# Optimization experiments

Measured on AMD Instinct MI355X. Metric: run time of the kernel, lower is better.

Reference implementation:

```python
import jax, jax.numpy as jnp
import numpy as np

S, B, NS, NC = 128, 64, 128, 8
D, Z, H, HI, NF = 32, 64, 128, 128, 2
N = NS * B
LOG2PI = float(np.log(2.0 * np.pi))
_m_in = np.arange(1, Z + 1)
_m_hid = (np.arange(HI) % (Z - 1)) + 1
MASK1 = jnp.asarray((_m_hid[None, :] >= _m_in[:, None]).astype(np.float32))  # [Z,HI]
MASK2 = jnp.asarray((_m_in[None, :] > _m_hid[:, None]).astype(np.float32))   # [HI,Z]


def setup_inputs() -> dict:
    key = jax.random.key(0)
    ks = jax.random.split(key, 16)
    r = lambda i, shape: jax.random.normal(ks[i], shape, jnp.float32) * 0.1
    return dict(
        input=jax.random.normal(ks[0], (S, B, D), jnp.float32),
        eps=jax.random.normal(ks[1], (S, N, Z), jnp.float32),
        u=jax.random.uniform(ks[2], (S, 3, NC, NS, B), dtype=jnp.float32),
        Wxh=r(3, (D, H)), Wzh=r(4, (Z, H)), bh=jnp.zeros(H, jnp.float32),
        Wg=r(5, (H, Z)), bg=jnp.zeros(Z, jnp.float32),
        Wp=r(6, (H, Z)), bp=jnp.zeros(Z, jnp.float32),
        Wz=r(7, (Z, Z)), bz=jnp.zeros(Z, jnp.float32),
        Wsc=r(8, (Z, Z)), bsc=jnp.zeros(Z, jnp.float32),
        iaf_W1=r(9, (NF, Z, HI)), iaf_b1=jnp.zeros((NF, HI), jnp.float32),
        iaf_Wm=r(10, (NF, HI, Z)), iaf_bm=jnp.zeros((NF, Z), jnp.float32),
        iaf_Ws=r(11, (NF, HI, Z)), iaf_bs=jnp.zeros((NF, Z), jnp.float32),
        We1=r(12, (Z, H)), be1=jnp.zeros(H, jnp.float32),
        We2=r(13, (H, 4 * NC)), be2=jnp.zeros(4 * NC, jnp.float32),
    )


def _forward(input, eps, u, Wxh, Wzh, bh, Wg, bg, Wp, bp, Wz, bz, Wsc, bsc,
             iaf_W1, iaf_b1, iaf_Wm, iaf_bm, iaf_Ws, iaf_bs, We1, be1, We2, be2):
    def step(z_prev, inp):
        x, eps_t, u_t = inp                        # x:[B,D] eps_t:[N,Z] u_t:[3,NC,NS,B]
        xr = jnp.tile(x, (NS, 1))                  # == input[i].repeat(n_samples, 1) -> [N,D]
        # GatedTransition
        h = jax.nn.relu(xr @ Wxh + z_prev @ Wzh + bh)
        gate = jax.nn.sigmoid(h @ Wg + bg)
        prop = h @ Wp + bp
        loc = (1.0 - gate) * (z_prev @ Wz + bz) + gate * prop
        scale = jax.nn.softplus(jax.nn.relu(prop) @ Wsc + bsc) + 1e-3
        # base rsample + log_prob of base sample (eps form)
        z = loc + scale * eps_t
        base_lp = jnp.sum(-0.5 * eps_t * eps_t - jnp.log(scale) - 0.5 * LOG2PI, axis=-1)
        # IAF stack: y = sigma*x + (1-sigma)*mu, cached log_prob = base_lp - sum log sigma
        logdet = jnp.zeros((N,), z.dtype)
        for f in range(NF):
            hh = jax.nn.relu(z @ (iaf_W1[f] * MASK1) + iaf_b1[f])
            mu = hh @ (iaf_Wm[f] * MASK2) + iaf_bm[f]
            sg = jax.nn.sigmoid(hh @ (iaf_Ws[f] * MASK2) + iaf_bs[f] + 1.0)
            z = sg * z + (1.0 - sg) * mu
            logdet = logdet + jnp.sum(jnp.log(sg), axis=-1)
        z_lp = (base_lp - logdet).reshape(NS, B)
        # Emitter -> [N, 4*NC]; .t().view(4,NC,NS,B).split([3,1])
        e = jax.nn.relu(z @ We1 + be1) @ We2 + be2
        et = e.T.reshape(4, NC, NS, B)
        logits, frac = et[:3], jax.nn.sigmoid(et[3:4])
        samp = (u_t < jax.nn.sigmoid(logits)).astype(jnp.float32)  # Bernoulli sample
        x_lp = samp * jax.nn.log_sigmoid(logits) + (1.0 - samp) * jax.nn.log_sigmoid(-logits)
        return z, (samp, frac, x_lp, z_lp)

    z0 = jnp.zeros((N, Z), input.dtype)
    _, (samples, fractions, x_logprobs, z_logprobs) = jax.lax.scan(step, z0, (input, eps, u))
    return samples, fractions, x_logprobs, z_logprobs


def reference(input, eps, u, Wxh, Wzh, bh, Wg, bg, Wp, bp, Wz, bz, Wsc, bsc,
              iaf_W1, iaf_b1, iaf_Wm, iaf_bm, iaf_Ws, iaf_bs, We1, be1, We2, be2):
    return _forward(input, eps, u, Wxh, Wzh, bh, Wg, bg, Wp, bp, Wz, bz, Wsc, bsc,
                    iaf_W1, iaf_b1, iaf_Wm, iaf_bm, iaf_Ws, iaf_bs, We1, be1, We2, be2)
```

## Files before the change

kernel.cpp:

```cpp
#include <hip/hip_runtime.h>


typedef _Float16 f16x8 __attribute__((ext_vector_type(8)));
typedef _Float16 f16x4 __attribute__((ext_vector_type(4)));
typedef float    f32x4 __attribute__((ext_vector_type(4)));
typedef unsigned short u16;
typedef unsigned long long u64;

#define MFMA16(a,b,c) __builtin_amdgcn_mfma_f32_16x16x32_f16((a),(b),(c),0,0,0)
#define FENCE() __builtin_amdgcn_sched_barrier(0)

namespace {
constexpr int S = 128;
constexpr long FRAC_OFF = 25165824L;
constexpr long XLP_OFF  = 33554432L;
constexpr long ZLP_OFF  = 58720256L;
constexpr float HLOG2PI = 0.91893853320467274f;
constexpr float INVLO   = 1.0f / 2048.0f;

constexpr int C1HI = 0,      C1LO = 12288;
constexpr int GPHI = 24576,  GPLO = 40960;
constexpr int WZHI = 57344,  WZLO = 61440;
constexpr int SCHI = 65536,  SCLO = 69632;
constexpr int W1B  = 73728;
constexpr int MSB  = 106496;
constexpr int E1HI = 172032, E1LO = 180224;
constexpr int E2HI = 188416, E2LO = 192512;
constexpr int XHI  = 196608, XLO  = 458752;
}

__device__ __forceinline__ float sigm(float x)      { return 1.0f / (1.0f + __expf(-x)); }
__device__ __forceinline__ float softplusf_(float x){ return fmaxf(x, 0.f) + __logf(1.f + __expf(-fabsf(x))); }
__device__ __forceinline__ float logsigm(float x)   { return fminf(x, 0.f) - __logf(1.f + __expf(-fabsf(x))); }

__device__ __forceinline__ void split2(float v, _Float16& hi, _Float16& lo) {
    hi = (_Float16)v;
    lo = (_Float16)((v - (float)hi) * 2048.0f);
}

__device__ __forceinline__ f16x8 rdA(const u16* t, int row, int k, int strideEls, int swm) {
    int byte = ((row * strideEls + k) * 2) ^ ((row & swm) << 4);
    return *(const f16x8*)((const char*)t + byte);
}
__device__ __forceinline__ f16x8 ldB(const u16* wa, int base, int col, int K, int koff) {
    return *(const f16x8*)(wa + base + col * K + koff);
}
__device__ __forceinline__ f16x8 ldLo(const u16* lds, int el, int col) {
    int byte = (el * 2) ^ ((col & 7) << 4);
    return *(const f16x8*)((const char*)lds + byte);
}

template<int NKS, int STRIDE, int SWM>
__device__ __forceinline__ void mmDual(const u16* Th, const u16* Tl, int lnc, int kf,
                                       const f16x8 (&wh)[NKS], const f16x8 (&wl)[NKS],
                                       float bias, f32x4& H0, f32x4& L0, f32x4& H1, f32x4& L1)
{
    H0 = (f32x4){bias, bias, bias, bias}; H1 = H0;
    L0 = (f32x4){0.f, 0.f, 0.f, 0.f};     L1 = L0;
#pragma unroll
    for (int ks = 0; ks < NKS; ++ks) {
        int k = ks * 32 + kf;
        f16x8 a0h = rdA(Th, lnc,      k, STRIDE, SWM);
        f16x8 a0l = rdA(Tl, lnc,      k, STRIDE, SWM);
        f16x8 a1h = rdA(Th, 16 + lnc, k, STRIDE, SWM);
        f16x8 a1l = rdA(Tl, 16 + lnc, k, STRIDE, SWM);
        H0 = MFMA16(a0h, wh[ks], H0); L0 = MFMA16(a0h, wl[ks], L0); L0 = MFMA16(a0l, wh[ks], L0);
        H1 = MFMA16(a1h, wh[ks], H1); L1 = MFMA16(a1h, wl[ks], L1); L1 = MFMA16(a1l, wh[ks], L1);
    }
}

template<bool RELU>
__device__ __forceinline__ void stAct(f32x4 H, f32x4 L, int rt, int lng, int col,
                                      u16* th, u16* tl, int strideEls, int swm)
{
#pragma unroll
    for (int q = 0; q < 4; ++q) {
        int row = rt * 16 + lng * 4 + q;
        float v = H[q] + L[q] * INVLO;
        if (RELU) v = fmaxf(v, 0.f);
        _Float16 hi, lo; split2(v, hi, lo);
        int byte = ((row * strideEls + col) * 2) ^ ((row & swm) << 4);
        *(_Float16*)((char*)th + byte) = hi;
        *(_Float16*)((char*)tl + byte) = lo;
    }
}
__device__ __forceinline__ void stScr(f32x4 H, f32x4 L, int rt, int lng, int col,
                                      float* s, int strideEls)
{
#pragma unroll
    for (int q = 0; q < 4; ++q) {
        int row = rt * 16 + lng * 4 + q;
        int byte = ((row * strideEls + col) * 4) ^ ((row & 7) << 4);
        *(float*)((char*)s + byte) = H[q] + L[q] * INVLO;
    }
}
__device__ __forceinline__ f32x4 rdS4(const float* s, int strideEls, int row, int c) {
    int byte = ((row * strideEls + c) * 4) ^ ((row & 7) << 4);
    return *(const f32x4*)((const char*)s + byte);
}
__device__ __forceinline__ float rdS1(const float* s, int strideEls, int row, int c) {
    int byte = ((row * strideEls + c) * 4) ^ ((row & 7) << 4);
    return *(const float*)((const char*)s + byte);
}
__device__ __forceinline__ void wrS4(float* s, int strideEls, int row, int c, f32x4 v) {
    int byte = ((row * strideEls + c) * 4) ^ ((row & 7) << 4);
    *(f32x4*)((char*)s + byte) = v;
}
__device__ __forceinline__ void wrF16x4(u16* t, int strideEls, int row, int c, f16x4 v) {
    int byte = ((row * strideEls + c) * 2) ^ ((row & 7) << 4);
    *(f16x4*)((char*)t + byte) = v;
}
__device__ __forceinline__ f16x4 rdF16x4(const u16* t, int strideEls, int row, int c) {
    int byte = ((row * strideEls + c) * 2) ^ ((row & 7) << 4);
    return *(const f16x4*)((const char*)t + byte);
}

__global__ void prep_kernel(const float* __restrict__ input,
                            const float* __restrict__ Wxh, const float* __restrict__ Wzh,
                            const float* __restrict__ Wg,  const float* __restrict__ Wp,
                            const float* __restrict__ Wz,  const float* __restrict__ Wsc,
                            const float* __restrict__ W1,  const float* __restrict__ Wm,
                            const float* __restrict__ Ws_, const float* __restrict__ We1,
                            const float* __restrict__ We2, u16* __restrict__ wa)
{
    int idx = blockIdx.x * 256 + threadIdx.x;
    if (idx < 98304) {
        int hio = 0, loo = 0; float v = 0.f;
        int i = idx;
        if (i < 12288) {
            int col = i / 96, k = i % 96;
            v = (k < 32) ? Wxh[k * 128 + col] : Wzh[(k - 32) * 128 + col];
            hio = C1HI + i; loo = C1LO + i;
        } else if (i < 28672) { int j = i - 12288;
            int col = j >> 7, k = j & 127;
            v = (col < 64) ? Wg[k * 64 + col] : Wp[k * 64 + col - 64];
            hio = GPHI + j; loo = GPLO + j;
        } else if (i < 32768) { int j = i - 28672;
            int col = j >> 6, k = j & 63; v = Wz[k * 64 + col];
            hio = WZHI + j; loo = WZLO + j;
        } else if (i < 36864) { int j = i - 32768;
            int col = j >> 6, k = j & 63; v = Wsc[k * 64 + col];
            hio = SCHI + j; loo = SCLO + j;
        } else if (i < 53248) { int j = i - 36864;
            int f = j >> 13, jj = j & 8191;
            int col = jj >> 6, k = jj & 63;
            v = W1[(f * 64 + k) * 128 + col] * (((col % 63) >= k) ? 1.f : 0.f);
            hio = W1B + f * 16384 + jj; loo = hio + 8192;
        } else if (i < 86016) { int j = i - 53248;
            int f = j >> 14, jj = j & 16383;
            int col = jj >> 7, k = jj & 127;
            if (col < 64) v = Wm[(f * 128 + k) * 64 + col] * (((k % 63) < col) ? 1.f : 0.f);
            else { int c = col - 64;
                   v = Ws_[(f * 128 + k) * 64 + c]         * (((k % 63) < c)   ? 1.f : 0.f); }
            hio = MSB + f * 32768 + jj; loo = hio + 16384;
        } else if (i < 94208) { int j = i - 86016;
            int col = j >> 6, k = j & 63; v = We1[k * 128 + col];
            hio = E1HI + j; loo = E1LO + j;
        } else { int j = i - 94208;
            int col = j >> 7, k = j & 127; v = We2[k * 32 + col];
            hio = E2HI + j; loo = E2LO + j;
        }
        _Float16 hi, lo; split2(v, hi, lo);
        wa[hio] = __builtin_bit_cast(u16, hi);
        wa[loo] = __builtin_bit_cast(u16, lo);
    } else {
        int j = idx - 98304;
        if (j < 262144) {
            float v = input[j];
            _Float16 hi, lo; split2(v, hi, lo);
            wa[XHI + j] = __builtin_bit_cast(u16, hi);
            wa[XLO + j] = __builtin_bit_cast(u16, lo);
        }
    }
}

__global__ __launch_bounds__(256, 1)
void ssm_mfma_kernel(const float* __restrict__ eps, const float* __restrict__ u,
                     const float* __restrict__ bh,  const float* __restrict__ bg,
                     const float* __restrict__ bp,  const float* __restrict__ bz,
                     const float* __restrict__ bsc, const float* __restrict__ b1,
                     const float* __restrict__ bm,  const float* __restrict__ bs,
                     const float* __restrict__ be1, const float* __restrict__ be2,
                     const u16* __restrict__ wa, float* __restrict__ out)
{
    __shared__ u16 tXh[32 * 32],  tXl[32 * 32];
    __shared__ u16 tZh[32 * 64],  tZl[32 * 64];
    __shared__ u16 tHh[32 * 128], tHl[32 * 128];
    __shared__ u16 tPh[32 * 64],  tPl[32 * 64];
    __shared__ float scrB[32 * 128];
    __shared__ float scrZ[32 * 64];
    __shared__ float lpS[32][9];
    __shared__ u16 loMS[32768];
    __shared__ u16 loGP[16384];

    const int tid = threadIdx.x;
    const int ln  = tid & 63, w = tid >> 6;
    const int lnc = ln & 15, lng = ln >> 4;
    const int r0  = blockIdx.x * 32, b0 = r0 & 63;
    const int kf  = lng * 8;
    const int ct0   = w * 32 + lnc;
    const int colz  = w * 16 + lnc;
    const int colE2 = (w & 1) * 16 + lnc;
    const int khE2  = w >> 1;
    const int crow  = tid >> 3, cc = (tid & 7) * 8;
    const int erow  = tid & 31, cg = (tid >> 5) * 4;

    for (int i8 = tid; i8 < 4096; i8 += 256) {
        int el = i8 * 8;
        int f = el >> 14, rem = el & 16383, col = rem >> 7;
        f16x8 v = *(const f16x8*)(wa + MSB + f * 32768 + 16384 + rem);
        int byte = (el * 2) ^ ((col & 7) << 4);
        *(f16x8*)((char*)loMS + byte) = v;
    }
    for (int i8 = tid; i8 < 2048; i8 += 256) {
        int el = i8 * 8;
        int col = el >> 7;
        f16x8 v = *(const f16x8*)(wa + GPLO + el);
        int byte = (el * 2) ^ ((col & 7) << 4);
        *(f16x8*)((char*)loGP + byte) = v;
    }

    f16x8 wC1h[2][3], wC1l[2][3];
    f16x8 wGPh[2][4];
    f16x8 wWZh[2], wWZl[2], wSCh[2], wSCl[2];
    f16x8 wW1h[2][2][2], wW1l[2][2][2];
    f16x8 wMSh[2][2][4];
    f16x8 wE1h[2][2], wE1l[2][2];
    f16x8 wE2h[2], wE2l[2];
#pragma unroll
    for (int j = 0; j < 2; ++j) {
        int colj = ct0 + j * 16;
#pragma unroll
        for (int ks = 0; ks < 3; ++ks) {
            wC1h[j][ks] = ldB(wa, C1HI, colj, 96, ks * 32 + kf);
            wC1l[j][ks] = ldB(wa, C1LO, colj, 96, ks * 32 + kf);
        }
#pragma unroll
        for (int ks = 0; ks < 4; ++ks)
            wGPh[j][ks] = ldB(wa, GPHI, colj, 128, ks * 32 + kf);
#pragma unroll
        for (int ks = 0; ks < 2; ++ks) {
            wE1h[j][ks] = ldB(wa, E1HI, colj, 64, ks * 32 + kf);
            wE1l[j][ks] = ldB(wa, E1LO, colj, 64, ks * 32 + kf);
        }
#pragma unroll
        for (int f = 0; f < 2; ++f) {
#pragma unroll
            for (int ks = 0; ks < 2; ++ks) {
                wW1h[f][j][ks] = ldB(wa, W1B + f * 16384,        colj, 64, ks * 32 + kf);
                wW1l[f][j][ks] = ldB(wa, W1B + f * 16384 + 8192, colj, 64, ks * 32 + kf);
            }
#pragma unroll
            for (int ks = 0; ks < 4; ++ks)
                wMSh[f][j][ks] = ldB(wa, MSB + f * 32768, colj, 128, ks * 32 + kf);
        }
    }
#pragma unroll
    for (int ks = 0; ks < 2; ++ks) {
        wWZh[ks] = ldB(wa, WZHI, colz, 64, ks * 32 + kf);
        wWZl[ks] = ldB(wa, WZLO, colz, 64, ks * 32 + kf);
        wSCh[ks] = ldB(wa, SCHI, colz, 64, ks * 32 + kf);
        wSCl[ks] = ldB(wa, SCLO, colz, 64, ks * 32 + kf);
        wE2h[ks] = ldB(wa, E2HI, colE2, 128, khE2 * 64 + ks * 32 + kf);
        wE2l[ks] = ldB(wa, E2LO, colE2, 128, khE2 * 64 + ks * 32 + kf);
    }

    float bhv[2], bGPv[2], bW1v[2][2], bMSv[2][2], bE1v[2];
#pragma unroll
    for (int j = 0; j < 2; ++j) {
        int colj = ct0 + j * 16;
        bhv[j]  = bh[colj];
        bGPv[j] = (colj < 64) ? bg[colj] : bp[colj - 64];
        bE1v[j] = be1[colj];
#pragma unroll
        for (int f = 0; f < 2; ++f) {
            bW1v[f][j] = b1[f * 128 + colj];
            bMSv[f][j] = (colj < 64) ? bm[f * 64 + colj] : bs[f * 64 + colj - 64];
        }
    }
    const float bzv  = bz[colz];
    const float bscv = bsc[colz];
    const float bE2v = (khE2 == 0) ? be2[colE2] : 0.f;

    for (int i = tid; i < 32 * 64; i += 256) { tZh[i] = 0; tZl[i] = 0; }
    {
        int rr = tid >> 3, d4 = (tid & 7) * 4;
        int ge = (b0 + rr) * 32 + d4;
        u64 xh = *(const u64*)(wa + XHI + ge);
        u64 xl = *(const u64*)(wa + XLO + ge);
        int byte = (rr * 64 + d4 * 2) ^ ((rr & 3) << 4);
        *(u64*)((char*)tXh + byte) = xh;
        *(u64*)((char*)tXl + byte) = xl;
    }
    FENCE();
    __syncthreads();
    FENCE();

    for (int t = 0; t < S; ++t) {
        f32x4 epsA, epsB;

        {
            f32x4 H[2], L[2], H1[2], L1[2];
#pragma unroll
            for (int j = 0; j < 2; ++j) {
                H[j]  = (f32x4){bhv[j], bhv[j], bhv[j], bhv[j]};
                H1[j] = H[j];
                L[j]  = (f32x4){0.f, 0.f, 0.f, 0.f};
                L1[j] = L[j];
            }
#pragma unroll
            for (int ks = 0; ks < 3; ++ks) {
                f16x8 a0h, a0l, a1h, a1l;
                if (ks == 0) {
                    a0h = rdA(tXh, lnc, kf, 32, 3);      a0l = rdA(tXl, lnc, kf, 32, 3);
                    a1h = rdA(tXh, 16 + lnc, kf, 32, 3); a1l = rdA(tXl, 16 + lnc, kf, 32, 3);
                } else {
                    int k = (ks - 1) * 32 + kf;
                    a0h = rdA(tZh, lnc, k, 64, 7);       a0l = rdA(tZl, lnc, k, 64, 7);
                    a1h = rdA(tZh, 16 + lnc, k, 64, 7);  a1l = rdA(tZl, 16 + lnc, k, 64, 7);
                }
#pragma unroll
                for (int j = 0; j < 2; ++j) {
                    H[j]  = MFMA16(a0h, wC1h[j][ks], H[j]);  L[j]  = MFMA16(a0h, wC1l[j][ks], L[j]);  L[j]  = MFMA16(a0l, wC1h[j][ks], L[j]);
                    H1[j] = MFMA16(a1h, wC1h[j][ks], H1[j]); L1[j] = MFMA16(a1h, wC1l[j][ks], L1[j]); L1[j] = MFMA16(a1l, wC1h[j][ks], L1[j]);
                }
            }
#pragma unroll
            for (int j = 0; j < 2; ++j) {
                stAct<true>(H[j],  L[j],  0, lng, ct0 + j * 16, tHh, tHl, 128, 7);
                stAct<true>(H1[j], L1[j], 1, lng, ct0 + j * 16, tHh, tHl, 128, 7);
            }
        }
        {
            f32x4 ZH0, ZL0, ZH1, ZL1;
            mmDual<2, 64, 7>(tZh, tZl, lnc, kf, wWZh, wWZl, bzv, ZH0, ZL0, ZH1, ZL1);
            stScr(ZH0, ZL0, 0, lng, colz, scrZ, 64);
            stScr(ZH1, ZL1, 1, lng, colz, scrZ, 64);
        }
        FENCE();
        __syncthreads();
        FENCE();

        {
            f32x4 H[2], L[2], H1[2], L1[2];
#pragma unroll
            for (int j = 0; j < 2; ++j) {
                H[j]  = (f32x4){bGPv[j], bGPv[j], bGPv[j], bGPv[j]};
                H1[j] = H[j];
                L[j]  = (f32x4){0.f, 0.f, 0.f, 0.f};
                L1[j] = L[j];
            }
#pragma unroll
            for (int ks = 0; ks < 4; ++ks) {
                int k = ks * 32 + kf;
                f16x8 a0h = rdA(tHh, lnc, k, 128, 7),      a0l = rdA(tHl, lnc, k, 128, 7);
                f16x8 a1h = rdA(tHh, 16 + lnc, k, 128, 7), a1l = rdA(tHl, 16 + lnc, k, 128, 7);
#pragma unroll
                for (int j = 0; j < 2; ++j) {
                    int colj = ct0 + j * 16;
                    f16x8 bhf = wGPh[j][ks];
                    f16x8 blf = ldLo(loGP, colj * 128 + k, colj);
                    H[j]  = MFMA16(a0h, bhf, H[j]);  L[j]  = MFMA16(a0h, blf, L[j]);  L[j]  = MFMA16(a0l, bhf, L[j]);
                    H1[j] = MFMA16(a1h, bhf, H1[j]); L1[j] = MFMA16(a1h, blf, L1[j]); L1[j] = MFMA16(a1l, bhf, L1[j]);
                }
            }
#pragma unroll
            for (int j = 0; j < 2; ++j) {
                stScr(H[j],  L[j],  0, lng, ct0 + j * 16, scrB, 128);
                stScr(H1[j], L1[j], 1, lng, ct0 + j * 16, scrB, 128);
            }
        }
        FENCE();
        __syncthreads();
        FENCE();

        {
            epsA = *(const f32x4*)(eps + ((size_t)t * 8192 + r0 + crow) * 64 + cc);
            epsB = *(const f32x4*)(eps + ((size_t)t * 8192 + r0 + crow) * 64 + cc + 4);
#pragma unroll
            for (int h4 = 0; h4 < 2; ++h4) {
                int c4 = cc + h4 * 4;
                f32x4 gp4 = rdS4(scrB, 128, crow, c4);
                f32x4 pr4 = rdS4(scrB, 128, crow, 64 + c4);
                f32x4 zw4 = rdS4(scrZ, 64, crow, c4);
                f32x4 loc4; f16x4 ph4, pl4;
#pragma unroll
                for (int i = 0; i < 4; ++i) {
                    float g = sigm(gp4[i]);
                    loc4[i] = (1.f - g) * zw4[i] + g * pr4[i];
                    float rp = fmaxf(pr4[i], 0.f);
                    _Float16 hi, lo; split2(rp, hi, lo); ph4[i] = hi; pl4[i] = lo;
                }
                wrS4(scrB, 128, crow, 64 + c4, loc4);
                wrF16x4(tPh, 64, crow, c4, ph4);
                wrF16x4(tPl, 64, crow, c4, pl4);
            }
        }
        FENCE();
        __syncthreads();
        FENCE();

        {
            f32x4 SH0, SL0, SH1, SL1;
            mmDual<2, 64, 7>(tPh, tPl, lnc, kf, wSCh, wSCl, bscv, SH0, SL0, SH1, SL1);
            stScr(SH0, SL0, 0, lng, colz, scrB, 128);
            stScr(SH1, SL1, 1, lng, colz, scrB, 128);
        }
        FENCE();
        __syncthreads();
        FENCE();

        float lp = 0.f;
#pragma unroll
        for (int h4 = 0; h4 < 2; ++h4) {
            int c4 = cc + h4 * 4;
            f32x4 ev   = (h4 == 0) ? epsA : epsB;
            f32x4 s4   = rdS4(scrB, 128, crow, c4);
            f32x4 loc4 = rdS4(scrB, 128, crow, 64 + c4);
            f16x4 zh4, zl4;
#pragma unroll
            for (int i = 0; i < 4; ++i) {
                float sc = softplusf_(s4[i]) + 0.001f;
                float zv = loc4[i] + sc * ev[i];
                lp += -0.5f * ev[i] * ev[i] - __logf(sc) - HLOG2PI;
                _Float16 hi, lo; split2(zv, hi, lo); zh4[i] = hi; zl4[i] = lo;
            }
            wrF16x4(tZh, 64, crow, c4, zh4);
            wrF16x4(tZl, 64, crow, c4, zl4);
        }
        FENCE();
        __syncthreads();
        FENCE();

#pragma unroll
        for (int f = 0; f < 2; ++f) {
            {
                f32x4 H[2], L[2], H1[2], L1[2];
#pragma unroll
                for (int j = 0; j < 2; ++j) {
                    H[j]  = (f32x4){bW1v[f][j], bW1v[f][j], bW1v[f][j], bW1v[f][j]};
                    H1[j] = H[j];
                    L[j]  = (f32x4){0.f, 0.f, 0.f, 0.f};
                    L1[j] = L[j];
                }
#pragma unroll
                for (int ks = 0; ks < 2; ++ks) {
                    int k = ks * 32 + kf;
                    f16x8 a0h = rdA(tZh, lnc, k, 64, 7),      a0l = rdA(tZl, lnc, k, 64, 7);
                    f16x8 a1h = rdA(tZh, 16 + lnc, k, 64, 7), a1l = rdA(tZl, 16 + lnc, k, 64, 7);
#pragma unroll
                    for (int j = 0; j < 2; ++j) {
                        H[j]  = MFMA16(a0h, wW1h[f][j][ks], H[j]);  L[j]  = MFMA16(a0h, wW1l[f][j][ks], L[j]);  L[j]  = MFMA16(a0l, wW1h[f][j][ks], L[j]);
                        H1[j] = MFMA16(a1h, wW1h[f][j][ks], H1[j]); L1[j] = MFMA16(a1h, wW1l[f][j][ks], L1[j]); L1[j] = MFMA16(a1l, wW1h[f][j][ks], L1[j]);
                    }
                }
#pragma unroll
                for (int j = 0; j < 2; ++j) {
                    stAct<true>(H[j],  L[j],  0, lng, ct0 + j * 16, tHh, tHl, 128, 7);
                    stAct<true>(H1[j], L1[j], 1, lng, ct0 + j * 16, tHh, tHl, 128, 7);
                }
            }
            FENCE();
            __syncthreads();
            FENCE();
            {
                f32x4 H[2], L[2], H1[2], L1[2];
#pragma unroll
                for (int j = 0; j < 2; ++j) {
                    H[j]  = (f32x4){bMSv[f][j], bMSv[f][j], bMSv[f][j], bMSv[f][j]};
                    H1[j] = H[j];
                    L[j]  = (f32x4){0.f, 0.f, 0.f, 0.f};
                    L1[j] = L[j];
                }
#pragma unroll
                for (int ks = 0; ks < 4; ++ks) {
                    int k = ks * 32 + kf;
                    f16x8 a0h = rdA(tHh, lnc, k, 128, 7),      a0l = rdA(tHl, lnc, k, 128, 7);
                    f16x8 a1h = rdA(tHh, 16 + lnc, k, 128, 7), a1l = rdA(tHl, 16 + lnc, k, 128, 7);
#pragma unroll
                    for (int j = 0; j < 2; ++j) {
                        int colj = ct0 + j * 16;
                        f16x8 bhf = wMSh[f][j][ks];
                        f16x8 blf = ldLo(loMS, f * 16384 + colj * 128 + k, colj);
                        H[j]  = MFMA16(a0h, bhf, H[j]);  L[j]  = MFMA16(a0h, blf, L[j]);  L[j]  = MFMA16(a0l, bhf, L[j]);
                        H1[j] = MFMA16(a1h, bhf, H1[j]); L1[j] = MFMA16(a1h, blf, L1[j]); L1[j] = MFMA16(a1l, bhf, L1[j]);
                    }
                }
#pragma unroll
                for (int j = 0; j < 2; ++j) {
                    stScr(H[j],  L[j],  0, lng, ct0 + j * 16, scrB, 128);
                    stScr(H1[j], L1[j], 1, lng, ct0 + j * 16, scrB, 128);
                }
            }
            FENCE();
            __syncthreads();
            FENCE();
            {
#pragma unroll
                for (int h4 = 0; h4 < 2; ++h4) {
                    int c4 = cc + h4 * 4;
                    f32x4 mu4 = rdS4(scrB, 128, crow, c4);
                    f32x4 sp4 = rdS4(scrB, 128, crow, 64 + c4);
                    f16x4 zh4 = rdF16x4(tZh, 64, crow, c4);
                    f16x4 zl4 = rdF16x4(tZl, 64, crow, c4);
                    f16x4 nzh, nzl;
#pragma unroll
                    for (int i = 0; i < 4; ++i) {
                        float zv = (float)zh4[i] + (float)zl4[i] * INVLO;
                        float sg = sigm(sp4[i] + 1.0f);
                        float zn = sg * zv + (1.f - sg) * mu4[i];
                        lp -= __logf(sg);
                        _Float16 hi, lo; split2(zn, hi, lo); nzh[i] = hi; nzl[i] = lo;
                    }
                    wrF16x4(tZh, 64, crow, c4, nzh);
                    wrF16x4(tZl, 64, crow, c4, nzl);
                }
                if (f == 1) lpS[crow][tid & 7] = lp;
            }
            FENCE();
            __syncthreads();
            FENCE();
        }

        {
            f32x4 H[2], L[2], H1[2], L1[2];
#pragma unroll
            for (int j = 0; j < 2; ++j) {
                H[j]  = (f32x4){bE1v[j], bE1v[j], bE1v[j], bE1v[j]};
                H1[j] = H[j];
                L[j]  = (f32x4){0.f, 0.f, 0.f, 0.f};
                L1[j] = L[j];
            }
#pragma unroll
            for (int ks = 0; ks < 2; ++ks) {
                int k = ks * 32 + kf;
                f16x8 a0h = rdA(tZh, lnc, k, 64, 7),      a0l = rdA(tZl, lnc, k, 64, 7);
                f16x8 a1h = rdA(tZh, 16 + lnc, k, 64, 7), a1l = rdA(tZl, 16 + lnc, k, 64, 7);
#pragma unroll
                for (int j = 0; j < 2; ++j) {
                    H[j]  = MFMA16(a0h, wE1h[j][ks], H[j]);  L[j]  = MFMA16(a0h, wE1l[j][ks], L[j]);  L[j]  = MFMA16(a0l, wE1h[j][ks], L[j]);
                    H1[j] = MFMA16(a1h, wE1h[j][ks], H1[j]); L1[j] = MFMA16(a1h, wE1l[j][ks], L1[j]); L1[j] = MFMA16(a1l, wE1h[j][ks], L1[j]);
                }
            }
#pragma unroll
            for (int j = 0; j < 2; ++j) {
                stAct<true>(H[j],  L[j],  0, lng, ct0 + j * 16, tHh, tHl, 128, 7);
                stAct<true>(H1[j], L1[j], 1, lng, ct0 + j * 16, tHh, tHl, 128, 7);
            }
        }
        FENCE();
        __syncthreads();
        FENCE();

        {
            f32x4 H0 = {bE2v, bE2v, bE2v, bE2v}, H1 = H0;
            f32x4 L0 = {0.f, 0.f, 0.f, 0.f},     L1 = L0;
#pragma unroll
            for (int ks = 0; ks < 2; ++ks) {
                int k = khE2 * 64 + ks * 32 + kf;
                f16x8 a0h = rdA(tHh, lnc, k, 128, 7),      a0l = rdA(tHl, lnc, k, 128, 7);
                f16x8 a1h = rdA(tHh, 16 + lnc, k, 128, 7), a1l = rdA(tHl, 16 + lnc, k, 128, 7);
                H0 = MFMA16(a0h, wE2h[ks], H0); L0 = MFMA16(a0h, wE2l[ks], L0); L0 = MFMA16(a0l, wE2h[ks], L0);
                H1 = MFMA16(a1h, wE2h[ks], H1); L1 = MFMA16(a1h, wE2l[ks], L1); L1 = MFMA16(a1l, wE2h[ks], L1);
            }
            stScr(H0, L0, 0, lng, khE2 * 64 + colE2, scrB, 128);
            stScr(H1, L1, 1, lng, khE2 * 64 + colE2, scrB, 128);
        }
        if (t + 1 < S) {
            int rr = tid >> 3, d4 = (tid & 7) * 4;
            int ge = ((t + 1) * 64 + b0 + rr) * 32 + d4;
            u64 xh = *(const u64*)(wa + XHI + ge);
            u64 xl = *(const u64*)(wa + XLO + ge);
            int byte = (rr * 64 + d4 * 2) ^ ((rr & 3) << 4);
            *(u64*)((char*)tXh + byte) = xh;
            *(u64*)((char*)tXl + byte) = xl;
        }
        FENCE();
        __syncthreads();
        FENCE();

        {
#pragma unroll
            for (int q = 0; q < 4; ++q) {
                int col = cg + q;
                float v = rdS1(scrB, 128, erow, col) + rdS1(scrB, 128, erow, 64 + col);
                if (col < 24) {
                    long plane = ((long)(t * 3 + (col >> 3)) * 8 + (col & 7)) * 8192 + r0 + erow;
                    float uvq = u[plane];
                    float sg = sigm(v);
                    bool hit = uvq < sg;
                    out[plane] = hit ? 1.f : 0.f;
                    out[XLP_OFF + plane] = hit ? logsigm(v) : logsigm(-v);
                } else {
                    long pf = ((long)t * 8 + (col & 7)) * 8192 + r0 + erow;
                    out[FRAC_OFF + pf] = sigm(v);
                }
            }
            if (tid < 32) {
                float s = 0.f;
#pragma unroll
                for (int g2 = 0; g2 < 8; ++g2) s += lpS[tid][g2];
                out[ZLP_OFF + (long)t * 8192 + r0 + tid] = s;
            }
        }
        FENCE();
    }
}

extern "C" void kernel_launch(void* const* d_in, const int* in_sizes, int n_in,
                              void* d_out, int out_size, void* d_ws, size_t ws_size,
                              hipStream_t stream)
{
    const float* input = (const float*)d_in[0];
    const float* eps   = (const float*)d_in[1];
    const float* u     = (const float*)d_in[2];
    const float* Wxh   = (const float*)d_in[3];
    const float* Wzh   = (const float*)d_in[4];
    const float* bh    = (const float*)d_in[5];
    const float* Wg    = (const float*)d_in[6];
    const float* bg    = (const float*)d_in[7];
    const float* Wp    = (const float*)d_in[8];
    const float* bp    = (const float*)d_in[9];
    const float* Wz    = (const float*)d_in[10];
    const float* bz    = (const float*)d_in[11];
    const float* Wsc   = (const float*)d_in[12];
    const float* bsc   = (const float*)d_in[13];
    const float* W1    = (const float*)d_in[14];
    const float* b1    = (const float*)d_in[15];
    const float* Wm    = (const float*)d_in[16];
    const float* bm    = (const float*)d_in[17];
    const float* Ws    = (const float*)d_in[18];
    const float* bs    = (const float*)d_in[19];
    const float* We1   = (const float*)d_in[20];
    const float* be1   = (const float*)d_in[21];
    const float* We2   = (const float*)d_in[22];
    const float* be2   = (const float*)d_in[23];

    u16* wa = (u16*)d_ws;

    hipLaunchKernelGGL(prep_kernel, dim3(1408), dim3(256), 0, stream,
                       input, Wxh, Wzh, Wg, Wp, Wz, Wsc, W1, Wm, Ws, We1, We2, wa);

    hipLaunchKernelGGL(ssm_mfma_kernel, dim3(256), dim3(256), 0, stream,
                       eps, u, bh, bg, bp, bz, bsc, b1, bm, bs, be1, be2,
                       wa, (float*)d_out);
}
```

Measured before the change: 2.642 ms.

## Split matmuls into per-row-tile passes and park weight fragments in AGPRs

```diff
diff --git a/kernel.cpp b/kernel.cpp
--- a/kernel.cpp
+++ b/kernel.cpp
@@ -9,6 +9,7 @@
 
 #define MFMA16(a,b,c) __builtin_amdgcn_mfma_f32_16x16x32_f16((a),(b),(c),0,0,0)
 #define FENCE() __builtin_amdgcn_sched_barrier(0)
+#define PARK(x) asm volatile("" : "+a"(x))
 
 namespace {
 constexpr int S = 128;
@@ -48,25 +49,6 @@
 __device__ __forceinline__ f16x8 ldLo(const u16* lds, int el, int col) {
     int byte = (el * 2) ^ ((col & 7) << 4);
     return *(const f16x8*)((const char*)lds + byte);
-}
-
-template<int NKS, int STRIDE, int SWM>
-__device__ __forceinline__ void mmDual(const u16* Th, const u16* Tl, int lnc, int kf,
-                                       const f16x8 (&wh)[NKS], const f16x8 (&wl)[NKS],
-                                       float bias, f32x4& H0, f32x4& L0, f32x4& H1, f32x4& L1)
-{
-    H0 = (f32x4){bias, bias, bias, bias}; H1 = H0;
-    L0 = (f32x4){0.f, 0.f, 0.f, 0.f};     L1 = L0;
-#pragma unroll
-    for (int ks = 0; ks < NKS; ++ks) {
-        int k = ks * 32 + kf;
-        f16x8 a0h = rdA(Th, lnc,      k, STRIDE, SWM);
-        f16x8 a0l = rdA(Tl, lnc,      k, STRIDE, SWM);
-        f16x8 a1h = rdA(Th, 16 + lnc, k, STRIDE, SWM);
-        f16x8 a1l = rdA(Tl, 16 + lnc, k, STRIDE, SWM);
-        H0 = MFMA16(a0h, wh[ks], H0); L0 = MFMA16(a0h, wl[ks], L0); L0 = MFMA16(a0l, wh[ks], L0);
-        H1 = MFMA16(a1h, wh[ks], H1); L1 = MFMA16(a1h, wl[ks], L1); L1 = MFMA16(a1l, wh[ks], L1);
-    }
 }
 
 template<bool RELU>
@@ -240,19 +222,20 @@
             wGPh[j][ks] = ldB(wa, GPHI, colj, 128, ks * 32 + kf);
 #pragma unroll
         for (int ks = 0; ks < 2; ++ks) {
-            wE1h[j][ks] = ldB(wa, E1HI, colj, 64, ks * 32 + kf);
-            wE1l[j][ks] = ldB(wa, E1LO, colj, 64, ks * 32 + kf);
+            wE1h[j][ks] = ldB(wa, E1HI, colj, 64, ks * 32 + kf); PARK(wE1h[j][ks]);
+            wE1l[j][ks] = ldB(wa, E1LO, colj, 64, ks * 32 + kf); PARK(wE1l[j][ks]);
         }
 #pragma unroll
         for (int f = 0; f < 2; ++f) {
 #pragma unroll
             for (int ks = 0; ks < 2; ++ks) {
-                wW1h[f][j][ks] = ldB(wa, W1B + f * 16384,        colj, 64, ks * 32 + kf);
-                wW1l[f][j][ks] = ldB(wa, W1B + f * 16384 + 8192, colj, 64, ks * 32 + kf);
-            }
-#pragma unroll
-            for (int ks = 0; ks < 4; ++ks)
-                wMSh[f][j][ks] = ldB(wa, MSB + f * 32768, colj, 128, ks * 32 + kf);
+                wW1h[f][j][ks] = ldB(wa, W1B + f * 16384,        colj, 64, ks * 32 + kf); PARK(wW1h[f][j][ks]);
+                wW1l[f][j][ks] = ldB(wa, W1B + f * 16384 + 8192, colj, 64, ks * 32 + kf); PARK(wW1l[f][j][ks]);
+            }
+#pragma unroll
+            for (int ks = 0; ks < 4; ++ks) {
+                wMSh[f][j][ks] = ldB(wa, MSB + f * 32768, colj, 128, ks * 32 + kf); PARK(wMSh[f][j][ks]);
+            }
         }
     }
 #pragma unroll
@@ -261,8 +244,8 @@
         wWZl[ks] = ldB(wa, WZLO, colz, 64, ks * 32 + kf);
         wSCh[ks] = ldB(wa, SCHI, colz, 64, ks * 32 + kf);
         wSCl[ks] = ldB(wa, SCLO, colz, 64, ks * 32 + kf);
-        wE2h[ks] = ldB(wa, E2HI, colE2, 128, khE2 * 64 + ks * 32 + kf);
-        wE2l[ks] = ldB(wa, E2LO, colE2, 128, khE2 * 64 + ks * 32 + kf);
+        wE2h[ks] = ldB(wa, E2HI, colE2, 128, khE2 * 64 + ks * 32 + kf); PARK(wE2h[ks]);
+        wE2l[ks] = ldB(wa, E2LO, colE2, 128, khE2 * 64 + ks * 32 + kf); PARK(wE2l[ks]);
     }
 
     float bhv[2], bGPv[2], bW1v[2][2], bMSv[2][2], bE1v[2];
@@ -299,78 +282,83 @@
     for (int t = 0; t < S; ++t) {
         f32x4 epsA, epsB;
 
-        {
-            f32x4 H[2], L[2], H1[2], L1[2];
+#pragma unroll
+        for (int rt = 0; rt < 2; ++rt) {
+            int arow = rt * 16 + lnc;
+            f32x4 H[2], L[2];
 #pragma unroll
             for (int j = 0; j < 2; ++j) {
-                H[j]  = (f32x4){bhv[j], bhv[j], bhv[j], bhv[j]};
-                H1[j] = H[j];
-                L[j]  = (f32x4){0.f, 0.f, 0.f, 0.f};
-                L1[j] = L[j];
+                H[j] = (f32x4){bhv[j], bhv[j], bhv[j], bhv[j]};
+                L[j] = (f32x4){0.f, 0.f, 0.f, 0.f};
             }
 #pragma unroll
             for (int ks = 0; ks < 3; ++ks) {
-                f16x8 a0h, a0l, a1h, a1l;
-                if (ks == 0) {
-                    a0h = rdA(tXh, lnc, kf, 32, 3);      a0l = rdA(tXl, lnc, kf, 32, 3);
-                    a1h = rdA(tXh, 16 + lnc, kf, 32, 3); a1l = rdA(tXl, 16 + lnc, kf, 32, 3);
-                } else {
+                f16x8 ah, al;
+                if (ks == 0) { ah = rdA(tXh, arow, kf, 32, 3); al = rdA(tXl, arow, kf, 32, 3); }
+                else {
                     int k = (ks - 1) * 32 + kf;
-                    a0h = rdA(tZh, lnc, k, 64, 7);       a0l = rdA(tZl, lnc, k, 64, 7);
-                    a1h = rdA(tZh, 16 + lnc, k, 64, 7);  a1l = rdA(tZl, 16 + lnc, k, 64, 7);
+                    ah = rdA(tZh, arow, k, 64, 7); al = rdA(tZl, arow, k, 64, 7);
                 }
 #pragma unroll
                 for (int j = 0; j < 2; ++j) {
-                    H[j]  = MFMA16(a0h, wC1h[j][ks], H[j]);  L[j]  = MFMA16(a0h, wC1l[j][ks], L[j]);  L[j]  = MFMA16(a0l, wC1h[j][ks], L[j]);
-                    H1[j] = MFMA16(a1h, wC1h[j][ks], H1[j]); L1[j] = MFMA16(a1h, wC1l[j][ks], L1[j]); L1[j] = MFMA16(a1l, wC1h[j][ks], L1[j]);
-                }
-            }
+                    H[j] = MFMA16(ah, wC1h[j][ks], H[j]);
+                    L[j] = MFMA16(ah, wC1l[j][ks], L[j]);
+                    L[j] = MFMA16(al, wC1h[j][ks], L[j]);
+                }
+            }
+#pragma unroll
+            for (int j = 0; j < 2; ++j)
+                stAct<true>(H[j], L[j], rt, lng, ct0 + j * 16, tHh, tHl, 128, 7);
+            FENCE();
+        }
+#pragma unroll
+        for (int rt = 0; rt < 2; ++rt) {
+            int arow = rt * 16 + lnc;
+            f32x4 ZH = {bzv, bzv, bzv, bzv};
+            f32x4 ZL = {0.f, 0.f, 0.f, 0.f};
+#pragma unroll
+            for (int ks = 0; ks < 2; ++ks) {
+                int k = ks * 32 + kf;
+                f16x8 ah = rdA(tZh, arow, k, 64, 7);
+                f16x8 al = rdA(tZl, arow, k, 64, 7);
+                ZH = MFMA16(ah, wWZh[ks], ZH);
+                ZL = MFMA16(ah, wWZl[ks], ZL);
+                ZL = MFMA16(al, wWZh[ks], ZL);
+            }
+            stScr(ZH, ZL, rt, lng, colz, scrZ, 64);
+            FENCE();
+        }
+        __syncthreads();
+        FENCE();
+
+#pragma unroll
+        for (int rt = 0; rt < 2; ++rt) {
+            int arow = rt * 16 + lnc;
+            f32x4 H[2], L[2];
 #pragma unroll
             for (int j = 0; j < 2; ++j) {
-                stAct<true>(H[j],  L[j],  0, lng, ct0 + j * 16, tHh, tHl, 128, 7);
-                stAct<true>(H1[j], L1[j], 1, lng, ct0 + j * 16, tHh, tHl, 128, 7);
-            }
-        }
-        {
-            f32x4 ZH0, ZL0, ZH1, ZL1;
-            mmDual<2, 64, 7>(tZh, tZl, lnc, kf, wWZh, wWZl, bzv, ZH0, ZL0, ZH1, ZL1);
-            stScr(ZH0, ZL0, 0, lng, colz, scrZ, 64);
-            stScr(ZH1, ZL1, 1, lng, colz, scrZ, 64);
-        }
-        FENCE();
-        __syncthreads();
-        FENCE();
-
-        {
-            f32x4 H[2], L[2], H1[2], L1[2];
-#pragma unroll
-            for (int j = 0; j < 2; ++j) {
-                H[j]  = (f32x4){bGPv[j], bGPv[j], bGPv[j], bGPv[j]};
-                H1[j] = H[j];
-                L[j]  = (f32x4){0.f, 0.f, 0.f, 0.f};
-                L1[j] = L[j];
+                H[j] = (f32x4){bGPv[j], bGPv[j], bGPv[j], bGPv[j]};
+                L[j] = (f32x4){0.f, 0.f, 0.f, 0.f};
             }
 #pragma unroll
             for (int ks = 0; ks < 4; ++ks) {
                 int k = ks * 32 + kf;
-                f16x8 a0h = rdA(tHh, lnc, k, 128, 7),      a0l = rdA(tHl, lnc, k, 128, 7);
-                f16x8 a1h = rdA(tHh, 16 + lnc, k, 128, 7), a1l = rdA(tHl, 16 + lnc, k, 128, 7);
+                f16x8 ah = rdA(tHh, arow, k, 128, 7);
+                f16x8 al = rdA(tHl, arow, k, 128, 7);
 #pragma unroll
                 for (int j = 0; j < 2; ++j) {
                     int colj = ct0 + j * 16;
-                    f16x8 bhf = wGPh[j][ks];
                     f16x8 blf = ldLo(loGP, colj * 128 + k, colj);
-                    H[j]  = MFMA16(a0h, bhf, H[j]);  L[j]  = MFMA16(a0h, blf, L[j]);  L[j]  = MFMA16(a0l, bhf, L[j]);
-                    H1[j] = MFMA16(a1h, bhf, H1[j]); L1[j] = MFMA16(a1h, blf, L1[j]); L1[j] = MFMA16(a1l, bhf, L1[j]);
-                }
-            }
-#pragma unroll
-            for (int j = 0; j < 2; ++j) {
-                stScr(H[j],  L[j],  0, lng, ct0 + j * 16, scrB, 128);
-                stScr(H1[j], L1[j], 1, lng, ct0 + j * 16, scrB, 128);
-            }
-        }
-        FENCE();
+                    H[j] = MFMA16(ah, wGPh[j][ks], H[j]);
+                    L[j] = MFMA16(ah, blf, L[j]);
+                    L[j] = MFMA16(al, wGPh[j][ks], L[j]);
+                }
+            }
+#pragma unroll
+            for (int j = 0; j < 2; ++j)
+                stScr(H[j], L[j], rt, lng, ct0 + j * 16, scrB, 128);
+            FENCE();
+        }
         __syncthreads();
         FENCE();
 
@@ -400,13 +388,23 @@
         __syncthreads();
         FENCE();
 
-        {
-            f32x4 SH0, SL0, SH1, SL1;
-            mmDual<2, 64, 7>(tPh, tPl, lnc, kf, wSCh, wSCl, bscv, SH0, SL0, SH1, SL1);
-            stScr(SH0, SL0, 0, lng, colz, scrB, 128);
-            stScr(SH1, SL1, 1, lng, colz, scrB, 128);
-        }
-        FENCE();
+#pragma unroll
+        for (int rt = 0; rt < 2; ++rt) {
+            int arow = rt * 16 + lnc;
+            f32x4 SH = {bscv, bscv, bscv, bscv};
+            f32x4 SL = {0.f, 0.f, 0.f, 0.f};
+#pragma unroll
+            for (int ks = 0; ks < 2; ++ks) {
+                int k = ks * 32 + kf;
+                f16x8 ah = rdA(tPh, arow, k, 64, 7);
+                f16x8 al = rdA(tPl, arow, k, 64, 7);
+                SH = MFMA16(ah, wSCh[ks], SH);
+                SL = MFMA16(ah, wSCl[ks], SL);
+                SL = MFMA16(al, wSCh[ks], SL);
+            }
+            stScr(SH, SL, rt, lng, colz, scrB, 128);
+            FENCE();
+        }
         __syncthreads();
         FENCE();
 
@@ -434,65 +432,62 @@
 
 #pragma unroll
         for (int f = 0; f < 2; ++f) {
-            {
-                f32x4 H[2], L[2], H1[2], L1[2];
+#pragma unroll
+            for (int rt = 0; rt < 2; ++rt) {
+                int arow = rt * 16 + lnc;
+                f32x4 H[2], L[2];
 #pragma unroll
                 for (int j = 0; j < 2; ++j) {
-                    H[j]  = (f32x4){bW1v[f][j], bW1v[f][j], bW1v[f][j], bW1v[f][j]};
-                    H1[j] = H[j];
-                    L[j]  = (f32x4){0.f, 0.f, 0.f, 0.f};
-                    L1[j] = L[j];
+                    H[j] = (f32x4){bW1v[f][j], bW1v[f][j], bW1v[f][j], bW1v[f][j]};
+                    L[j] = (f32x4){0.f, 0.f, 0.f, 0.f};
                 }
 #pragma unroll
                 for (int ks = 0; ks < 2; ++ks) {
                     int k = ks * 32 + kf;
-                    f16x8 a0h = rdA(tZh, lnc, k, 64, 7),      a0l = rdA(tZl, lnc, k, 64, 7);
-                    f16x8 a1h = rdA(tZh, 16 + lnc, k, 64, 7), a1l = rdA(tZl, 16 + lnc, k, 64, 7);
+                    f16x8 ah = rdA(tZh, arow, k, 64, 7);
+                    f16x8 al = rdA(tZl, arow, k, 64, 7);
 #pragma unroll
                     for (int j = 0; j < 2; ++j) {
-                        H[j]  = MFMA16(a0h, wW1h[f][j][ks], H[j]);  L[j]  = MFMA16(a0h, wW1l[f][j][ks], L[j]);  L[j]  = MFMA16(a0l, wW1h[f][j][ks], L[j]);
-                        H1[j] = MFMA16(a1h, wW1h[f][j][ks], H1[j]); L1[j] = MFMA16(a1h, wW1l[f][j][ks], L1[j]); L1[j] = MFMA16(a1l, wW1h[f][j][ks], L1[j]);
+                        H[j] = MFMA16(ah, wW1h[f][j][ks], H[j]);
+                        L[j] = MFMA16(ah, wW1l[f][j][ks], L[j]);
+                        L[j] = MFMA16(al, wW1h[f][j][ks], L[j]);
                     }
                 }
 #pragma unroll
+                for (int j = 0; j < 2; ++j)
+                    stAct<true>(H[j], L[j], rt, lng, ct0 + j * 16, tHh, tHl, 128, 7);
+                FENCE();
+            }
+            __syncthreads();
+            FENCE();
+#pragma unroll
+            for (int rt = 0; rt < 2; ++rt) {
+                int arow = rt * 16 + lnc;
+                f32x4 H[2], L[2];
+#pragma unroll
                 for (int j = 0; j < 2; ++j) {
-                    stAct<true>(H[j],  L[j],  0, lng, ct0 + j * 16, tHh, tHl, 128, 7);
-                    stAct<true>(H1[j], L1[j], 1, lng, ct0 + j * 16, tHh, tHl, 128, 7);
-                }
-            }
-            FENCE();
-            __syncthreads();
-            FENCE();
-            {
-                f32x4 H[2], L[2], H1[2], L1[2];
-#pragma unroll
-                for (int j = 0; j < 2; ++j) {
-                    H[j]  = (f32x4){bMSv[f][j], bMSv[f][j], bMSv[f][j], bMSv[f][j]};
-                    H1[j] = H[j];
-                    L[j]  = (f32x4){0.f, 0.f, 0.f, 0.f};
-                    L1[j] = L[j];
+                    H[j] = (f32x4){bMSv[f][j], bMSv[f][j], bMSv[f][j], bMSv[f][j]};
+                    L[j] = (f32x4){0.f, 0.f, 0.f, 0.f};
                 }
 #pragma unroll
                 for (int ks = 0; ks < 4; ++ks) {
                     int k = ks * 32 + kf;
-                    f16x8 a0h = rdA(tHh, lnc, k, 128, 7),      a0l = rdA(tHl, lnc, k, 128, 7);
-                    f16x8 a1h = rdA(tHh, 16 + lnc, k, 128, 7), a1l = rdA(tHl, 16 + lnc, k, 128, 7);
+                    f16x8 ah = rdA(tHh, arow, k, 128, 7);
+                    f16x8 al = rdA(tHl, arow, k, 128, 7);
 #pragma unroll
                     for (int j = 0; j < 2; ++j) {
                         int colj = ct0 + j * 16;
-                        f16x8 bhf = wMSh[f][j][ks];
                         f16x8 blf = ldLo(loMS, f * 16384 + colj * 128 + k, colj);
-                        H[j]  = MFMA16(a0h, bhf, H[j]);  L[j]  = MFMA16(a0h, blf, L[j]);  L[j]  = MFMA16(a0l, bhf, L[j]);
-                        H1[j] = MFMA16(a1h, bhf, H1[j]); L1[j] = MFMA16(a1h, blf, L1[j]); L1[j] = MFMA16(a1l, bhf, L1[j]);
+                        H[j] = MFMA16(ah, wMSh[f][j][ks], H[j]);
+                        L[j] = MFMA16(ah, blf, L[j]);
+                        L[j] = MFMA16(al, wMSh[f][j][ks], L[j]);
                     }
                 }
 #pragma unroll
-                for (int j = 0; j < 2; ++j) {
-                    stScr(H[j],  L[j],  0, lng, ct0 + j * 16, scrB, 128);
-                    stScr(H1[j], L1[j], 1, lng, ct0 + j * 16, scrB, 128);
-                }
-            }
-            FENCE();
+                for (int j = 0; j < 2; ++j)
+                    stScr(H[j], L[j], rt, lng, ct0 + j * 16, scrB, 128);
+                FENCE();
+            }
             __syncthreads();
             FENCE();
             {
@@ -522,49 +517,51 @@
             FENCE();
         }
 
-        {
-            f32x4 H[2], L[2], H1[2], L1[2];
+#pragma unroll
+        for (int rt = 0; rt < 2; ++rt) {
+            int arow = rt * 16 + lnc;
+            f32x4 H[2], L[2];
 #pragma unroll
             for (int j = 0; j < 2; ++j) {
-                H[j]  = (f32x4){bE1v[j], bE1v[j], bE1v[j], bE1v[j]};
-                H1[j] = H[j];
-                L[j]  = (f32x4){0.f, 0.f, 0.f, 0.f};
-                L1[j] = L[j];
+                H[j] = (f32x4){bE1v[j], bE1v[j], bE1v[j], bE1v[j]};
+                L[j] = (f32x4){0.f, 0.f, 0.f, 0.f};
             }
 #pragma unroll
             for (int ks = 0; ks < 2; ++ks) {
                 int k = ks * 32 + kf;
-                f16x8 a0h = rdA(tZh, lnc, k, 64, 7),      a0l = rdA(tZl, lnc, k, 64, 7);
-                f16x8 a1h = rdA(tZh, 16 + lnc, k, 64, 7), a1l = rdA(tZl, 16 + lnc, k, 64, 7);
+                f16x8 ah = rdA(tZh, arow, k, 64, 7);
+                f16x8 al = rdA(tZl, arow, k, 64, 7);
 #pragma unroll
                 for (int j = 0; j < 2; ++j) {
-                    H[j]  = MFMA16(a0h, wE1h[j][ks], H[j]);  L[j]  = MFMA16(a0h, wE1l[j][ks], L[j]);  L[j]  = MFMA16(a0l, wE1h[j][ks], L[j]);
-                    H1[j] = MFMA16(a1h, wE1h[j][ks], H1[j]); L1[j] = MFMA16(a1h, wE1l[j][ks], L1[j]); L1[j] = MFMA16(a1l, wE1h[j][ks], L1[j]);
-                }
-            }
-#pragma unroll
-            for (int j = 0; j < 2; ++j) {
-                stAct<true>(H[j],  L[j],  0, lng, ct0 + j * 16, tHh, tHl, 128, 7);
-                stAct<true>(H1[j], L1[j], 1, lng, ct0 + j * 16, tHh, tHl, 128, 7);
-            }
-        }
-        FENCE();
+                    H[j] = MFMA16(ah, wE1h[j][ks], H[j]);
+                    L[j] = MFMA16(ah, wE1l[j][ks], L[j]);
+                    L[j] = MFMA16(al, wE1h[j][ks], L[j]);
+                }
+            }
+#pragma unroll
+            for (int j = 0; j < 2; ++j)
+                stAct<true>(H[j], L[j], rt, lng, ct0 + j * 16, tHh, tHl, 128, 7);
+            FENCE();
+        }
         __syncthreads();
         FENCE();
 
-        {
-            f32x4 H0 = {bE2v, bE2v, bE2v, bE2v}, H1 = H0;
-            f32x4 L0 = {0.f, 0.f, 0.f, 0.f},     L1 = L0;
+#pragma unroll
+        for (int rt = 0; rt < 2; ++rt) {
+            int arow = rt * 16 + lnc;
+            f32x4 H = {bE2v, bE2v, bE2v, bE2v};
+            f32x4 L = {0.f, 0.f, 0.f, 0.f};
 #pragma unroll
             for (int ks = 0; ks < 2; ++ks) {
                 int k = khE2 * 64 + ks * 32 + kf;
-                f16x8 a0h = rdA(tHh, lnc, k, 128, 7),      a0l = rdA(tHl, lnc, k, 128, 7);
-                f16x8 a1h = rdA(tHh, 16 + lnc, k, 128, 7), a1l = rdA(tHl, 16 + lnc, k, 128, 7);
-                H0 = MFMA16(a0h, wE2h[ks], H0); L0 = MFMA16(a0h, wE2l[ks], L0); L0 = MFMA16(a0l, wE2h[ks], L0);
-                H1 = MFMA16(a1h, wE2h[ks], H1); L1 = MFMA16(a1h, wE2l[ks], L1); L1 = MFMA16(a1l, wE2h[ks], L1);
-            }
-            stScr(H0, L0, 0, lng, khE2 * 64 + colE2, scrB, 128);
-            stScr(H1, L1, 1, lng, khE2 * 64 + colE2, scrB, 128);
+                f16x8 ah = rdA(tHh, arow, k, 128, 7);
+                f16x8 al = rdA(tHl, arow, k, 128, 7);
+                H = MFMA16(ah, wE2h[ks], H);
+                L = MFMA16(ah, wE2l[ks], L);
+                L = MFMA16(al, wE2h[ks], L);
+            }
+            stScr(H, L, rt, lng, khE2 * 64 + colE2, scrB, 128);
+            FENCE();
         }
         if (t + 1 < S) {
             int rr = tid >> 3, d4 = (tid & 7) * 4;
```

Measured after the change: 3.478 ms. 31.6% more time.
